# Optimization experiments

Hardware: AMD Instinct MI355X
Metric: run time of the kernel (lower is better)

The kernel has to match this reference:

```python
import jax, jax.numpy as jnp
import numpy as np

H, W = 1024, 1024
NUM_FEATURES = 64
NUM_PILLARS = 100000


def setup_inputs() -> dict:
    key = jax.random.key(0)
    k1, k2 = jax.random.split(key)
    pillar_features = jax.random.normal(k1, (NUM_PILLARS, NUM_FEATURES), dtype=jnp.float32)
    coords = jax.random.randint(k2, (NUM_PILLARS, 3), 0, 1024, dtype=jnp.int64)
    return {"pillar_features": pillar_features, "coords": coords}


def reference(pillar_features, coords):
    # pillar_features: [N, F]; coords: [N, 3] = (batch_idx, y_idx, x_idx)
    x_idx = coords[:, 2]
    y_idx = coords[:, 1]
    valid = (x_idx >= 0) & (x_idx < W) & (y_idx >= 0) & (y_idx < H)
    # Flatten spatial dims; route invalid pillars to an out-of-bounds slot
    # that mode='drop' discards (matches the torch valid_mask filtering).
    flat_idx = jnp.where(valid, y_idx * W + x_idx, H * W)
    img = jnp.zeros((NUM_FEATURES, H * W), dtype=pillar_features.dtype)
    # single vectorized scatter: [F, N] updates into [F, H*W]
    img = img.at[:, flat_idx].set(pillar_features.T, mode='drop')
    return img.reshape(1, NUM_FEATURES, H, W)
```

## Files before the change

### kernel.cpp

```cpp
#include <hip/hip_runtime.h>


constexpr int H    = 1024;
constexpr int W    = 1024;
constexpr int HW   = H * W;
constexpr int NF   = 64;
constexpr int TILE = 256;
constexpr int HALF = 32;

typedef float nt4 __attribute__((ext_vector_type(4)));

__global__ void winner_kernel(const int* __restrict__ coords,
                              int* __restrict__ winner, int np) {
    int p = blockIdx.x * blockDim.x + threadIdx.x;
    if (p >= np) return;
    int y = coords[p * 3 + 1];
    int x = coords[p * 3 + 2];
    if ((unsigned)x < (unsigned)W && (unsigned)y < (unsigned)H) {
        atomicMax(winner + (y * W + x), p);
    }
}

__global__ void __launch_bounds__(256) fill_kernel(const float* __restrict__ feat,
                                                   const int* __restrict__ winner,
                                                   float* __restrict__ out) {
    __shared__ float lds[HALF * TILE];

    const int base = blockIdx.x * TILE;
    const int t    = threadIdx.x;
    const int wp   = winner[base + t];
    const int wv   = t >> 6;
    const int l    = t & 63;

    const float4* row = (const float4*)(feat + (size_t)max(wp, 0) * NF);

#pragma unroll
    for (int h = 0; h < 2; ++h) {
        if (wp >= 0) {
#pragma unroll
            for (int j = 0; j < 8; ++j) {
                float4 r = row[h * 8 + j];
                lds[(j * 4 + 0) * TILE + t] = r.x;
                lds[(j * 4 + 1) * TILE + t] = r.y;
                lds[(j * 4 + 2) * TILE + t] = r.z;
                lds[(j * 4 + 3) * TILE + t] = r.w;
            }
        } else {
#pragma unroll
            for (int j = 0; j < HALF; ++j) lds[j * TILE + t] = 0.0f;
        }
        __syncthreads();

#pragma unroll
        for (int p = 0; p < 8; ++p) {
            const int floc = p * 4 + wv;
            nt4 v = *(const nt4*)&lds[floc * TILE + l * 4];
            __builtin_nontemporal_store(
                v, (nt4*)(out + (size_t)(h * HALF + floc) * HW + base + l * 4));
        }
        __syncthreads();
    }
}

extern "C" void kernel_launch(void* const* d_in, const int* in_sizes, int n_in,
                              void* d_out, int out_size, void* d_ws, size_t ws_size,
                              hipStream_t stream) {
    const float* feat   = (const float*)d_in[0];
    const int*   coords = (const int*)d_in[1];
    float*       out    = (float*)d_out;
    int np = in_sizes[1] / 3;

    int* winner = (int*)d_ws;

    (void)hipMemsetAsync(winner, 0xFF, (size_t)HW * sizeof(int), stream);
    winner_kernel<<<(np + 255) / 256, 256, 0, stream>>>(coords, winner, np);
    fill_kernel<<<HW / TILE, 256, 0, stream>>>(feat, winner, out);
}
```

Baseline: 300.0 us.

## Software-pipeline feature gathers with LDS transposes across two tiles per block

Each block now handles two 256-pixel tiles. It prefetches the next half-row or next tile's gathered features into registers while the current LDS tile is stored. Branchy zero-fill is replaced by a select on loaded values, and __syncthreads is replaced by a lighter lgkmcnt wait plus s_barrier. The aim is to hide gather latency behind the output stores. The cost is more registers and half as many blocks.

```diff
diff --git a/kernel.cpp b/kernel.cpp
--- a/kernel.cpp
+++ b/kernel.cpp
@@ -7,6 +7,7 @@
 constexpr int NF   = 64;
 constexpr int TILE = 256;
 constexpr int HALF = 32;
+constexpr int TPB  = 2;
 
 typedef float nt4 __attribute__((ext_vector_type(4)));
 
@@ -21,44 +22,79 @@
     }
 }
 
+__device__ __forceinline__ void bar_lds() {
+    asm volatile("s_waitcnt lgkmcnt(0)" ::: "memory");
+    __builtin_amdgcn_s_barrier();
+}
+
 __global__ void __launch_bounds__(256) fill_kernel(const float* __restrict__ feat,
                                                    const int* __restrict__ winner,
                                                    float* __restrict__ out) {
     __shared__ float lds[HALF * TILE];
+    const int t  = threadIdx.x;
+    const int wv = t >> 6;
+    const int l  = t & 63;
 
-    const int base = blockIdx.x * TILE;
-    const int t    = threadIdx.x;
-    const int wp   = winner[base + t];
-    const int wv   = t >> 6;
-    const int l    = t & 63;
+    const int base = blockIdx.x * (TILE * TPB);
 
+    const float4 z4 = make_float4(0.f, 0.f, 0.f, 0.f);
+    float4 r[8];
+
+    int wp = winner[base + t];
     const float4* row = (const float4*)(feat + (size_t)max(wp, 0) * NF);
+    bool valid = wp >= 0;
+#pragma unroll
+    for (int j = 0; j < 8; ++j) { float4 v = row[j]; r[j] = valid ? v : z4; }
+
+    for (int tile = 0; tile < TPB; ++tile) {
+        const int tb = base + tile * TILE;
 
 #pragma unroll
-    for (int h = 0; h < 2; ++h) {
-        if (wp >= 0) {
+        for (int j = 0; j < 8; ++j) {
+            lds[(4 * j + 0) * TILE + t] = r[j].x;
+            lds[(4 * j + 1) * TILE + t] = r[j].y;
+            lds[(4 * j + 2) * TILE + t] = r[j].z;
+            lds[(4 * j + 3) * TILE + t] = r[j].w;
+        }
+        bar_lds();
+
 #pragma unroll
-            for (int j = 0; j < 8; ++j) {
-                float4 r = row[h * 8 + j];
-                lds[(j * 4 + 0) * TILE + t] = r.x;
-                lds[(j * 4 + 1) * TILE + t] = r.y;
-                lds[(j * 4 + 2) * TILE + t] = r.z;
-                lds[(j * 4 + 3) * TILE + t] = r.w;
-            }
-        } else {
+        for (int j = 0; j < 8; ++j) { float4 v = row[8 + j]; r[j] = valid ? v : z4; }
+
 #pragma unroll
-            for (int j = 0; j < HALF; ++j) lds[j * TILE + t] = 0.0f;
+        for (int p = 0; p < 8; ++p) {
+            const int f = p * 4 + wv;
+            nt4 v = *(const nt4*)&lds[f * TILE + l * 4];
+            __builtin_nontemporal_store(
+                v, (nt4*)(out + (size_t)f * HW + tb + l * 4));
         }
-        __syncthreads();
+        bar_lds();
+
+#pragma unroll
+        for (int j = 0; j < 8; ++j) {
+            lds[(4 * j + 0) * TILE + t] = r[j].x;
+            lds[(4 * j + 1) * TILE + t] = r[j].y;
+            lds[(4 * j + 2) * TILE + t] = r[j].z;
+            lds[(4 * j + 3) * TILE + t] = r[j].w;
+        }
+        bar_lds();
+
+        if (tile + 1 < TPB) {
+            wp    = winner[base + (tile + 1) * TILE + t];
+            row   = (const float4*)(feat + (size_t)max(wp, 0) * NF);
+            valid = wp >= 0;
+#pragma unroll
+            for (int j = 0; j < 8; ++j) { float4 v = row[j]; r[j] = valid ? v : z4; }
+        }
 
 #pragma unroll
         for (int p = 0; p < 8; ++p) {
             const int floc = p * 4 + wv;
             nt4 v = *(const nt4*)&lds[floc * TILE + l * 4];
             __builtin_nontemporal_store(
-                v, (nt4*)(out + (size_t)(h * HALF + floc) * HW + base + l * 4));
+                v, (nt4*)(out + (size_t)(HALF + floc) * HW + tb + l * 4));
         }
-        __syncthreads();
+        if (tile + 1 < TPB) bar_lds();
     }
 }
 
@@ -74,5 +110,5 @@
 
     (void)hipMemsetAsync(winner, 0xFF, (size_t)HW * sizeof(int), stream);
     winner_kernel<<<(np + 255) / 256, 256, 0, stream>>>(coords, winner, np);
-    fill_kernel<<<HW / TILE, 256, 0, stream>>>(feat, winner, out);
+    fill_kernel<<<HW / (TILE * TPB), 256, 0, stream>>>(feat, winner, out);
 }
```

Result: no change. 304.5 us (+1.5%).

## Restructure fill kernel into wider tiles with register double-buffered feature gathers

Applied to the files above, without the earlier changes.

Each block of the fill kernel now covers 2048 pixels instead of 256 and walks the 64 features in 16 chunks of 4. The next chunk's float4 gathers are prefetched into registers while the current chunk is written through LDS and stored with nontemporal stores. Barriers use a raw s_waitcnt lgkmcnt(0) plus s_barrier instead of __syncthreads. The aim is to overlap the scattered feature reads with the streaming writes and to give each wave longer contiguous stores. The cost is 8x fewer blocks (512), which lowers the parallelism available to hide latency, and more barriers per block.

```diff
diff --git a/kernel.cpp b/kernel.cpp
--- a/kernel.cpp
+++ b/kernel.cpp
@@ -5,8 +5,10 @@
 constexpr int W    = 1024;
 constexpr int HW   = H * W;
 constexpr int NF   = 64;
-constexpr int TILE = 256;
-constexpr int HALF = 32;
+constexpr int TILE = 2048;
+constexpr int CPT  = TILE / 256;
+constexpr int FP   = 4;
+constexpr int NP   = NF / FP;
 
 typedef float nt4 __attribute__((ext_vector_type(4)));
 
@@ -21,44 +23,67 @@
     }
 }
 
+__device__ __forceinline__ void bar_lds() {
+    asm volatile("s_waitcnt lgkmcnt(0)" ::: "memory");
+    __builtin_amdgcn_s_barrier();
+}
+
 __global__ void __launch_bounds__(256) fill_kernel(const float* __restrict__ feat,
                                                    const int* __restrict__ winner,
                                                    float* __restrict__ out) {
-    __shared__ float lds[HALF * TILE];
+    __shared__ float lds[FP * TILE];
+    const int t  = threadIdx.x;
+    const int wv = t >> 6;
+    const int l  = t & 63;
+    const int tb = blockIdx.x * TILE;
 
-    const int base = blockIdx.x * TILE;
-    const int t    = threadIdx.x;
-    const int wp   = winner[base + t];
-    const int wv   = t >> 6;
-    const int l    = t & 63;
+    const float4 z4 = make_float4(0.f, 0.f, 0.f, 0.f);
 
-    const float4* row = (const float4*)(feat + (size_t)max(wp, 0) * NF);
+    const float4* row[CPT];
+    bool          ok[CPT];
+#pragma unroll
+    for (int k = 0; k < CPT; ++k) {
+        int wp = winner[tb + k * 256 + t];
+        ok[k]  = wp >= 0;
+        row[k] = (const float4*)(feat + (size_t)max(wp, 0) * NF);
+    }
+
+    float4 g[2][CPT];
+#pragma unroll
+    for (int k = 0; k < CPT; ++k) {
+        float4 v = row[k][0];
+        g[0][k] = ok[k] ? v : z4;
+    }
 
 #pragma unroll
-    for (int h = 0; h < 2; ++h) {
-        if (wp >= 0) {
-#pragma unroll
-            for (int j = 0; j < 8; ++j) {
-                float4 r = row[h * 8 + j];
-                lds[(j * 4 + 0) * TILE + t] = r.x;
-                lds[(j * 4 + 1) * TILE + t] = r.y;
-                lds[(j * 4 + 2) * TILE + t] = r.z;
-                lds[(j * 4 + 3) * TILE + t] = r.w;
-            }
-        } else {
-#pragma unroll
-            for (int j = 0; j < HALF; ++j) lds[j * TILE + t] = 0.0f;
-        }
-        __syncthreads();
+    for (int p = 0; p < NP; ++p) {
+        const int cur = p & 1;
 
 #pragma unroll
-        for (int p = 0; p < 8; ++p) {
-            const int floc = p * 4 + wv;
-            nt4 v = *(const nt4*)&lds[floc * TILE + l * 4];
-            __builtin_nontemporal_store(
-                v, (nt4*)(out + (size_t)(h * HALF + floc) * HW + base + l * 4));
+        for (int k = 0; k < CPT; ++k) {
+            const int cc = k * 256 + t;
+            lds[0 * TILE + cc] = g[cur][k].x;
+            lds[1 * TILE + cc] = g[cur][k].y;
+            lds[2 * TILE + cc] = g[cur][k].z;
+            lds[3 * TILE + cc] = g[cur][k].w;
         }
-        __syncthreads();
+        bar_lds();
+
+        if (p + 1 < NP) {
+#pragma unroll
+            for (int k = 0; k < CPT; ++k) {
+                float4 v = row[k][p + 1];
+                g[cur ^ 1][k] = ok[k] ? v : z4;
+            }
+        }
+
+        float* dst = out + (size_t)(p * FP + wv) * HW + tb;
+#pragma unroll
+        for (int j = 0; j < TILE / 256; ++j) {
+            nt4 v = *(const nt4*)&lds[wv * TILE + j * 256 + l * 4];
+            __builtin_nontemporal_store(v, (nt4*)(dst + j * 256 + l * 4));
+        }
+        bar_lds();
     }
 }
 
```

Measured after the change: 295.7 us. Within noise of the previous version (-1.4%).
